# Performance work log

Hardware: AMD Instinct MI355X
Metric: run time of the kernel (lower is better)

Reference implementation:

```python
import jax, jax.numpy as jnp
import numpy as np

B, N_DOWN, N_UP, C_IN, C_OUT, SPIRAL, NNZ = 8, 12288, 49152, 64, 32, 9, 147456


def setup_inputs() -> dict:
    key = jax.random.key(0)
    ks = jax.random.split(key, 7)
    x = jax.random.normal(ks[0], (B, N_DOWN, C_IN), dtype=jnp.float32)
    up_rows = jax.random.randint(ks[1], (NNZ,), 0, N_UP, dtype=jnp.int32)
    up_cols = jax.random.randint(ks[2], (NNZ,), 0, N_DOWN, dtype=jnp.int32)
    up_vals = jax.random.uniform(ks[3], (NNZ,), dtype=jnp.float32)
    spiral_indices = jax.random.randint(ks[4], (N_UP, SPIRAL), 0, N_UP, dtype=jnp.int32)
    weight = jax.random.normal(ks[5], (C_OUT, SPIRAL * C_IN), dtype=jnp.float32) * 0.02
    bias = jax.random.normal(ks[6], (C_OUT,), dtype=jnp.float32) * 0.02
    return {"x": x, "up_rows": up_rows, "up_cols": up_cols, "up_vals": up_vals,
            "spiral_indices": spiral_indices, "weight": weight, "bias": bias}


def reference(x, up_rows, up_cols, up_vals, spiral_indices, weight, bias):
    # Pool: sparse upsample matmul along vertex dim (dim=1)
    # gathered: [B, nnz, C_in]
    gathered = x[:, up_cols, :] * up_vals[None, :, None]
    pooled = jax.vmap(lambda g: jax.ops.segment_sum(g, up_rows, num_segments=N_UP))(gathered)  # [B, N_up, C_in]
    # SpiralConv: gather spiral neighbors, flatten, linear
    flat_idx = spiral_indices.reshape(-1)  # [N_up*SPIRAL]
    g = pooled[:, flat_idx, :].reshape(B, N_UP, SPIRAL * C_IN)
    out = jnp.einsum('bnk,ok->bno', g, weight) + bias
    return jax.nn.relu(out)
```

## Files before the change

kernel.cpp:

```cpp
#include <hip/hip_runtime.h>
#include <hip/hip_bf16.h>

#define BB 8
#define ND 12288
#define NU 49152
#define CI 64
#define CO 32
#define SP 9
#define NNZ 147456
#define KTOT (SP * CI)
#define KPAD 584

using short8 = __attribute__((ext_vector_type(8))) short;
using f32x4  = __attribute__((ext_vector_type(4))) float;

#define OFF_WBF   ((size_t)BB * NU * CI * 2)
#define OFF_CNT   (OFF_WBF   + (size_t)CO * KTOT * 2)
#define OFF_START (OFF_CNT   + (size_t)NU * 4)
#define OFF_FILL  (OFF_START + (size_t)(NU + 1) * 4 + 4)
#define OFF_PENT  (OFF_FILL  + (size_t)NU * 4)

static __device__ __forceinline__ unsigned short f2bf(float f) {
    __hip_bfloat16 h = __float2bfloat16(f);
    return *reinterpret_cast<unsigned short*>(&h);
}

__global__ __launch_bounds__(256) void hist_kernel(
    const int* __restrict__ rows, int* __restrict__ cnt)
{
    const int i = blockIdx.x * 256 + threadIdx.x;
    atomicAdd(&cnt[rows[i]], 1);
}

__global__ __launch_bounds__(1024) void scan_kernel(
    const int* __restrict__ cnt, int* __restrict__ start, int* __restrict__ fill)
{
    __shared__ int wsum[16], woff[16];
    const int t = threadIdx.x, lane = t & 63, w = t >> 6;
    const int base = t * 48;
    int c[48];
    int s = 0;
#pragma unroll
    for (int i = 0; i < 48; ++i) { c[i] = cnt[base + i]; s += c[i]; }
    int incl = s;
#pragma unroll
    for (int d = 1; d < 64; d <<= 1) {
        const int v = __shfl_up(incl, d, 64);
        if (lane >= d) incl += v;
    }
    if (lane == 63) wsum[w] = incl;
    __syncthreads();
    if (w == 0 && lane < 16) {
        const int v = wsum[lane];
        int inc2 = v;
#pragma unroll
        for (int d = 1; d < 16; d <<= 1) {
            const int u = __shfl_up(inc2, d, 16);
            if (lane >= d) inc2 += u;
        }
        woff[lane] = inc2 - v;
    }
    __syncthreads();
    int run = woff[w] + incl - s;
#pragma unroll
    for (int i = 0; i < 48; ++i) {
        start[base + i] = run;
        fill[base + i]  = run;
        run += c[i];
    }
    if (t == 1023) start[NU] = run;
}

__global__ __launch_bounds__(256) void perm_kernel(
    const int* __restrict__ rows, const int* __restrict__ cols,
    const float* __restrict__ vals, int* __restrict__ fill,
    int2* __restrict__ pent)
{
    const int i = blockIdx.x * 256 + threadIdx.x;
    const int pos = atomicAdd(&fill[rows[i]], 1);
    int2 e;
    e.x = cols[i];
    e.y = __float_as_int(vals[i]);
    pent[pos] = e;
}

__global__ __launch_bounds__(256) void wcvt_kernel(
    const float* __restrict__ weight, unsigned short* __restrict__ wbf)
{
    const int i = blockIdx.x * 256 + threadIdx.x;
    wbf[i] = f2bf(weight[i]);
}

__global__ __launch_bounds__(256) void pool_kernel(
    const float* __restrict__ x, const int* __restrict__ start,
    const int2* __restrict__ pent, unsigned short* __restrict__ pooled)
{
    const int t   = blockIdx.x * 256 + threadIdx.x;
    const int row = t >> 4;
    const int cq  = (t & 15) << 2;
    const int s = start[row], e = start[row + 1];
    float4 acc[BB];
#pragma unroll
    for (int b = 0; b < BB; ++b) acc[b] = make_float4(0.f, 0.f, 0.f, 0.f);

    int j = s;
    for (; j + 1 < e; j += 2) {
        const int2 e0 = pent[j], e1 = pent[j + 1];
        const float v0 = __int_as_float(e0.y), v1 = __int_as_float(e1.y);
        float4 xv0[BB], xv1[BB];
#pragma unroll
        for (int b = 0; b < BB; ++b)
            xv0[b] = *(const float4*)(x + ((size_t)(b * ND + e0.x) * CI + cq));
#pragma unroll
        for (int b = 0; b < BB; ++b)
            xv1[b] = *(const float4*)(x + ((size_t)(b * ND + e1.x) * CI + cq));
        __builtin_amdgcn_sched_barrier(0);
#pragma unroll
        for (int b = 0; b < BB; ++b) {
            acc[b].x = fmaf(v0, xv0[b].x, acc[b].x);
            acc[b].y = fmaf(v0, xv0[b].y, acc[b].y);
            acc[b].z = fmaf(v0, xv0[b].z, acc[b].z);
            acc[b].w = fmaf(v0, xv0[b].w, acc[b].w);
            acc[b].x = fmaf(v1, xv1[b].x, acc[b].x);
            acc[b].y = fmaf(v1, xv1[b].y, acc[b].y);
            acc[b].z = fmaf(v1, xv1[b].z, acc[b].z);
            acc[b].w = fmaf(v1, xv1[b].w, acc[b].w);
        }
    }
    if (j < e) {
        const int2 e0 = pent[j];
        const float v0 = __int_as_float(e0.y);
#pragma unroll
        for (int b = 0; b < BB; ++b) {
            const float4 xv = *(const float4*)(x + ((size_t)(b * ND + e0.x) * CI + cq));
            acc[b].x = fmaf(v0, xv.x, acc[b].x);
            acc[b].y = fmaf(v0, xv.y, acc[b].y);
            acc[b].z = fmaf(v0, xv.z, acc[b].z);
            acc[b].w = fmaf(v0, xv.w, acc[b].w);
        }
    }
#pragma unroll
    for (int b = 0; b < BB; ++b) {
        uint2 pk;
        pk.x = (unsigned)f2bf(acc[b].x) | ((unsigned)f2bf(acc[b].y) << 16);
        pk.y = (unsigned)f2bf(acc[b].z) | ((unsigned)f2bf(acc[b].w) << 16);
        *(uint2*)(pooled + ((size_t)row * BB + b) * CI + cq) = pk;
    }
}

__global__ __launch_bounds__(512) void conv_mfma(
    const unsigned short* __restrict__ pooled, const unsigned short* __restrict__ wbf,
    const int* __restrict__ spiral, const float* __restrict__ bias,
    float* __restrict__ out)
{
    __shared__ __align__(16) unsigned short wT[CO][KPAD];

    const int tid  = threadIdx.x;
    const int b    = tid >> 6;
    const int lane = tid & 63;
    const int r    = lane & 15;
    const int kg   = lane >> 4;
    const int n0   = blockIdx.x * 16;
    const int n    = n0 + r;

    {
        const int o = tid >> 4;
        const int c = tid & 15;
#pragma unroll
        for (int j = 0; j < 9; ++j) {
            const int idx = (j * 16 + c) * 4;
            *(uint2*)&wT[o][idx] = *(const uint2*)(wbf + (size_t)o * KTOT + idx);
        }
    }

    int g[SP];
#pragma unroll
    for (int s = 0; s < SP; ++s) g[s] = spiral[n * SP + s];

    const unsigned short* abase = pooled + (size_t)b * CI + (size_t)kg * 8;

    short8 a0l,a0h,a1l,a1h,a2l,a2h,a3l,a3h,a4l,a4h,a5l,a5h,a6l,a6h,a7l,a7h,a8l,a8h;
#define LDA(vl, vh, s) \
    vl = *(const short8*)(abase + (size_t)g[s] * (BB * CI)); \
    vh = *(const short8*)(abase + (size_t)g[s] * (BB * CI) + 32)
    LDA(a0l,a0h,0); LDA(a1l,a1h,1); LDA(a2l,a2h,2); LDA(a3l,a3h,3);
    LDA(a4l,a4h,4); LDA(a5l,a5h,5); LDA(a6l,a6h,6); LDA(a7l,a7h,7);
    LDA(a8l,a8h,8);
#undef LDA
    __builtin_amdgcn_sched_barrier(0);

    __syncthreads();

    f32x4 acc0 = {0.f, 0.f, 0.f, 0.f};
    f32x4 acc1 = {0.f, 0.f, 0.f, 0.f};
    const unsigned short* w0 = &wT[r][kg * 8];
    const unsigned short* w1 = &wT[16 + r][kg * 8];

#define STEP(al, ah, s) do { \
    const short8 b00 = *(const short8*)(w0 + (s) * 64); \
    const short8 b01 = *(const short8*)(w1 + (s) * 64); \
    const short8 b10 = *(const short8*)(w0 + (s) * 64 + 32); \
    const short8 b11 = *(const short8*)(w1 + (s) * 64 + 32); \
    acc0 = __builtin_amdgcn_mfma_f32_16x16x32_bf16(al, b00, acc0, 0, 0, 0); \
    acc1 = __builtin_amdgcn_mfma_f32_16x16x32_bf16(al, b01, acc1, 0, 0, 0); \
    acc0 = __builtin_amdgcn_mfma_f32_16x16x32_bf16(ah, b10, acc0, 0, 0, 0); \
    acc1 = __builtin_amdgcn_mfma_f32_16x16x32_bf16(ah, b11, acc1, 0, 0, 0); \
  } while (0)
    STEP(a0l,a0h,0); STEP(a1l,a1h,1); STEP(a2l,a2h,2); STEP(a3l,a3h,3);
    STEP(a4l,a4h,4); STEP(a5l,a5h,5); STEP(a6l,a6h,6); STEP(a7l,a7h,7);
    STEP(a8l,a8h,8);
#undef STEP

    const float bo0 = bias[r];
    const float bo1 = bias[16 + r];
    const size_t mbase = (size_t)b * NU + n0 + kg * 4;
#pragma unroll
    for (int reg = 0; reg < 4; ++reg) {
        const size_t m = mbase + reg;
        __builtin_nontemporal_store(fmaxf(acc0[reg] + bo0, 0.f), out + m * CO + r);
        __builtin_nontemporal_store(fmaxf(acc1[reg] + bo1, 0.f), out + m * CO + 16 + r);
    }
}

extern "C" void kernel_launch(void* const* d_in, const int* in_sizes, int n_in,
                              void* d_out, int out_size, void* d_ws, size_t ws_size,
                              hipStream_t stream) {
    const float* x      = (const float*)d_in[0];
    const int*   rows   = (const int*)d_in[1];
    const int*   cols   = (const int*)d_in[2];
    const float* vals   = (const float*)d_in[3];
    const int*   spiral = (const int*)d_in[4];
    const float* weight = (const float*)d_in[5];
    const float* bias   = (const float*)d_in[6];
    float*       out    = (float*)d_out;

    char* ws = (char*)d_ws;
    unsigned short* pooled = (unsigned short*)ws;
    unsigned short* wbf    = (unsigned short*)(ws + OFF_WBF);
    int*   cnt    = (int*)(ws + OFF_CNT);
    int*   startp = (int*)(ws + OFF_START);
    int*   fill   = (int*)(ws + OFF_FILL);
    int2*  pent   = (int2*)(ws + OFF_PENT);

    hipMemsetAsync(cnt, 0, (size_t)NU * 4, stream);

    hist_kernel<<<NNZ / 256, 256, 0, stream>>>(rows, cnt);
    scan_kernel<<<1, 1024, 0, stream>>>(cnt, startp, fill);
    perm_kernel<<<NNZ / 256, 256, 0, stream>>>(rows, cols, vals, fill, pent);
    wcvt_kernel<<<(CO * KTOT) / 256, 256, 0, stream>>>(weight, wbf);
    pool_kernel<<<(NU * 16) / 256, 256, 0, stream>>>(x, startp, pent, pooled);

    conv_mfma<<<NU / 16, 512, 0, stream>>>(pooled, wbf, spiral, bias, out);
}
```

Before: 245.8 us.

## Pre-convert x to bf16 vertex-major layout and fuse prep into one kernel

Adds a prep kernel that converts x to bf16 in a [vertex][batch][channel] layout, converts the weights, and zeroes the histogram counters. This replaces the memset and the separate weight-conversion kernel. The pool kernel now gathers one contiguous 1 KB bf16 row per nonzero instead of eight scattered fp32 rows, which halves gather bytes and improves locality. The cost is an extra full pass over x, plus bf16 rounding of the inputs before accumulation. Output stores also switch from nontemporal to regular stores.

```diff
diff --git a/kernel.cpp b/kernel.cpp
--- a/kernel.cpp
+++ b/kernel.cpp
@@ -19,10 +19,45 @@
 #define OFF_START (OFF_CNT   + (size_t)NU * 4)
 #define OFF_FILL  (OFF_START + (size_t)(NU + 1) * 4 + 4)
 #define OFF_PENT  (OFF_FILL  + (size_t)NU * 4)
+#define OFF_XBF   (((OFF_PENT + (size_t)NNZ * 8) + 15) & ~(size_t)15)
 
 static __device__ __forceinline__ unsigned short f2bf(float f) {
     __hip_bfloat16 h = __float2bfloat16(f);
     return *reinterpret_cast<unsigned short*>(&h);
+}
+static __device__ __forceinline__ unsigned pk2(float a, float b) {
+    return (unsigned)f2bf(a) | ((unsigned)f2bf(b) << 16);
+}
+static __device__ __forceinline__ float bflo(unsigned u) { return __uint_as_float(u << 16); }
+static __device__ __forceinline__ float bfhi(unsigned u) { return __uint_as_float(u & 0xffff0000u); }
+
+__global__ __launch_bounds__(256) void prep_kernel(
+    const float* __restrict__ x, const float* __restrict__ weight,
+    unsigned short* __restrict__ xbf2, unsigned short* __restrict__ wbf,
+    int* __restrict__ cnt)
+{
+    const int i = blockIdx.x * 256 + threadIdx.x;
+    {
+        const int b  = i / (ND * 8);
+        const int r  = i - b * (ND * 8);
+        const int n  = r >> 3;
+        const int c8 = r & 7;
+        const float4* px = (const float4*)(x + (((size_t)b * ND + n) * CI + c8 * 8));
+        const float4 v0 = px[0], v1 = px[1];
+        uint4 q;
+        q.x = pk2(v0.x, v0.y); q.y = pk2(v0.z, v0.w);
+        q.z = pk2(v1.x, v1.y); q.w = pk2(v1.z, v1.w);
+        *(uint4*)(xbf2 + ((size_t)n * BB + b) * CI + c8 * 8) = q;
+    }
+    if (i < NU) cnt[i] = 0;
+    if (i < (CO * KTOT) / 8) {
+        const float4* pw = (const float4*)(weight + (size_t)i * 8);
+        const float4 v0 = pw[0], v1 = pw[1];
+        uint4 q;
+        q.x = pk2(v0.x, v0.y); q.y = pk2(v0.z, v0.w);
+        q.z = pk2(v1.x, v1.y); q.w = pk2(v1.z, v1.w);
+        *(uint4*)(wbf + (size_t)i * 8) = q;
+    }
 }
 
 __global__ __launch_bounds__(256) void hist_kernel(
@@ -84,68 +119,51 @@
     pent[pos] = e;
 }
 
-__global__ __launch_bounds__(256) void wcvt_kernel(
-    const float* __restrict__ weight, unsigned short* __restrict__ wbf)
-{
-    const int i = blockIdx.x * 256 + threadIdx.x;
-    wbf[i] = f2bf(weight[i]);
-}
-
 __global__ __launch_bounds__(256) void pool_kernel(
-    const float* __restrict__ x, const int* __restrict__ start,
+    const unsigned short* __restrict__ xbf2, const int* __restrict__ start,
     const int2* __restrict__ pent, unsigned short* __restrict__ pooled)
 {
-    const int t   = blockIdx.x * 256 + threadIdx.x;
-    const int row = t >> 4;
-    const int cq  = (t & 15) << 2;
+    const int tid  = threadIdx.x;
+    const int row  = blockIdx.x * 4 + (tid >> 6);
+    const int lane = tid & 63;
+    const int b    = lane >> 3;
+    const int c8   = lane & 7;
     const int s = start[row], e = start[row + 1];
-    float4 acc[BB];
-#pragma unroll
-    for (int b = 0; b < BB; ++b) acc[b] = make_float4(0.f, 0.f, 0.f, 0.f);
+
+    const unsigned short* xb = xbf2 + (size_t)b * CI + c8 * 8;
+    float acc[8];
+#pragma unroll
+    for (int k = 0; k < 8; ++k) acc[k] = 0.f;
+
+#define ACC8(q, v) do { \
+    acc[0] = fmaf(v, bflo(q.x), acc[0]); acc[1] = fmaf(v, bfhi(q.x), acc[1]); \
+    acc[2] = fmaf(v, bflo(q.y), acc[2]); acc[3] = fmaf(v, bfhi(q.y), acc[3]); \
+    acc[4] = fmaf(v, bflo(q.z), acc[4]); acc[5] = fmaf(v, bfhi(q.z), acc[5]); \
+    acc[6] = fmaf(v, bflo(q.w), acc[6]); acc[7] = fmaf(v, bfhi(q.w), acc[7]); \
+  } while (0)
 
     int j = s;
     for (; j + 1 < e; j += 2) {
         const int2 e0 = pent[j], e1 = pent[j + 1];
         const float v0 = __int_as_float(e0.y), v1 = __int_as_float(e1.y);
-        float4 xv0[BB], xv1[BB];
-#pragma unroll
-        for (int b = 0; b < BB; ++b)
-            xv0[b] = *(const float4*)(x + ((size_t)(b * ND + e0.x) * CI + cq));
-#pragma unroll
-        for (int b = 0; b < BB; ++b)
-            xv1[b] = *(const float4*)(x + ((size_t)(b * ND + e1.x) * CI + cq));
+        const uint4 q0 = *(const uint4*)(xb + (size_t)e0.x * (BB * CI));
+        const uint4 q1 = *(const uint4*)(xb + (size_t)e1.x * (BB * CI));
         __builtin_amdgcn_sched_barrier(0);
-#pragma unroll
-        for (int b = 0; b < BB; ++b) {
-            acc[b].x = fmaf(v0, xv0[b].x, acc[b].x);
-            acc[b].y = fmaf(v0, xv0[b].y, acc[b].y);
-            acc[b].z = fmaf(v0, xv0[b].z, acc[b].z);
-            acc[b].w = fmaf(v0, xv0[b].w, acc[b].w);
-            acc[b].x = fmaf(v1, xv1[b].x, acc[b].x);
-            acc[b].y = fmaf(v1, xv1[b].y, acc[b].y);
-            acc[b].z = fmaf(v1, xv1[b].z, acc[b].z);
-            acc[b].w = fmaf(v1, xv1[b].w, acc[b].w);
-        }
+        ACC8(q0, v0);
+        ACC8(q1, v1);
     }
     if (j < e) {
         const int2 e0 = pent[j];
         const float v0 = __int_as_float(e0.y);
-#pragma unroll
-        for (int b = 0; b < BB; ++b) {
-            const float4 xv = *(const float4*)(x + ((size_t)(b * ND + e0.x) * CI + cq));
-            acc[b].x = fmaf(v0, xv.x, acc[b].x);
-            acc[b].y = fmaf(v0, xv.y, acc[b].y);
-            acc[b].z = fmaf(v0, xv.z, acc[b].z);
-            acc[b].w = fmaf(v0, xv.w, acc[b].w);
-        }
-    }
-#pragma unroll
-    for (int b = 0; b < BB; ++b) {
-        uint2 pk;
-        pk.x = (unsigned)f2bf(acc[b].x) | ((unsigned)f2bf(acc[b].y) << 16);
-        pk.y = (unsigned)f2bf(acc[b].z) | ((unsigned)f2bf(acc[b].w) << 16);
-        *(uint2*)(pooled + ((size_t)row * BB + b) * CI + cq) = pk;
-    }
+        const uint4 q0 = *(const uint4*)(xb + (size_t)e0.x * (BB * CI));
+        ACC8(q0, v0);
+    }
+#undef ACC8
+
+    uint4 o;
+    o.x = pk2(acc[0], acc[1]); o.y = pk2(acc[2], acc[3]);
+    o.z = pk2(acc[4], acc[5]); o.w = pk2(acc[6], acc[7]);
+    *(uint4*)(pooled + ((size_t)row * BB + b) * CI + c8 * 8) = o;
 }
 
 __global__ __launch_bounds__(512) void conv_mfma(
@@ -217,8 +235,8 @@
 #pragma unroll
     for (int reg = 0; reg < 4; ++reg) {
         const size_t m = mbase + reg;
-        __builtin_nontemporal_store(fmaxf(acc0[reg] + bo0, 0.f), out + m * CO + r);
-        __builtin_nontemporal_store(fmaxf(acc1[reg] + bo1, 0.f), out + m * CO + 16 + r);
+        out[m * CO + r]      = fmaxf(acc0[reg] + bo0, 0.f);
+        out[m * CO + 16 + r] = fmaxf(acc1[reg] + bo1, 0.f);
     }
 }
 
@@ -241,14 +259,13 @@
     int*   startp = (int*)(ws + OFF_START);
     int*   fill   = (int*)(ws + OFF_FILL);
     int2*  pent   = (int2*)(ws + OFF_PENT);
-
-    hipMemsetAsync(cnt, 0, (size_t)NU * 4, stream);
-
+    unsigned short* xbf2 = (unsigned short*)(ws + OFF_XBF);
+
+    prep_kernel<<<(BB * ND * 8) / 256, 256, 0, stream>>>(x, weight, xbf2, wbf, cnt);
     hist_kernel<<<NNZ / 256, 256, 0, stream>>>(rows, cnt);
     scan_kernel<<<1, 1024, 0, stream>>>(cnt, startp, fill);
     perm_kernel<<<NNZ / 256, 256, 0, stream>>>(rows, cols, vals, fill, pent);
-    wcvt_kernel<<<(CO * KTOT) / 256, 256, 0, stream>>>(weight, wbf);
-    pool_kernel<<<(NU * 16) / 256, 256, 0, stream>>>(x, startp, pent, pooled);
+    pool_kernel<<<NU / 4, 256, 0, stream>>>(xbf2, startp, pent, pooled);
 
     conv_mfma<<<NU / 16, 512, 0, stream>>>(pooled, wbf, spiral, bias, out);
 }
```

Result: faster. 224.2 us (-8.8%).
